# Kernel optimization log

Measured on AMD Instinct MI355X. Metric: run time of the kernel, lower is better.

## Reference

```python
import jax, jax.numpy as jnp
import numpy as np

B, H, W, C = 32, 56, 56, 256
WS = 7            # window size (hard-coded 49=7*7 in original topk modules)
NH = 8            # num heads
HD = C // NH      # head dim = 32
KCH = HD // 2     # channel top-k = 16
KSPT = 28         # spatial top-k
N = WS * WS       # 49 tokens per window
SCALE = HD ** -0.5
MLP_H = 4 * C

def _rel_index(ws):
    coords = np.stack(np.meshgrid(np.arange(ws), np.arange(ws), indexing='ij')).reshape(2, -1)
    rc = (coords[:, :, None] - coords[:, None, :]).transpose(1, 2, 0).astype(np.int64)
    rc[:, :, 0] += ws - 1
    rc[:, :, 1] += ws - 1
    rc[:, :, 0] *= 2 * ws - 1
    return jnp.asarray(rc.sum(-1))  # (N, N)

REL_IDX = _rel_index(WS)

def setup_inputs():
    key = jax.random.key(0)
    ks = jax.random.split(key, 10)
    p = lambda k, shp: jax.random.normal(k, shp, jnp.float32) * 0.02
    return dict(
        x=jax.random.normal(ks[0], (B, H * W, C), jnp.float32),
        norm1_g=jnp.ones((C,), jnp.float32), norm1_b=jnp.zeros((C,), jnp.float32),
        wq=p(ks[1], (C, C)), bq=jnp.zeros((C,), jnp.float32),
        wk=p(ks[2], (C // 2, C // 2)), bk=jnp.zeros((C // 2,), jnp.float32),
        wv=p(ks[3], (C, C)), bv=jnp.zeros((C,), jnp.float32),
        wproj=p(ks[4], (C, C)), bproj=jnp.zeros((C,), jnp.float32),
        wch=p(ks[5], (2 * HD, HD)), bch=jnp.zeros((HD,), jnp.float32),
        rpb_table=p(ks[6], ((2 * WS - 1) ** 2, NH)),
        norm2_g=jnp.ones((C,), jnp.float32), norm2_b=jnp.zeros((C,), jnp.float32),
        w1=p(ks[7], (C, MLP_H)), b1=jnp.zeros((MLP_H,), jnp.float32),
        w2=p(ks[8], (MLP_H, C)), b2=jnp.zeros((C,), jnp.float32),
    )

def _ln(x, g, b):
    mu = x.mean(-1, keepdims=True)
    var = x.var(-1, keepdims=True)
    return (x - mu) / jnp.sqrt(var + 1e-5) * g + b

def reference(x, norm1_g, norm1_b, wq, bq, wk, bk, wv, bv, wproj, bproj,
              wch, bch, rpb_table, norm2_g, norm2_b, w1, b1, w2, b2):
    shortcut = x
    xn = _ln(x, norm1_g, norm1_b).reshape(B, H, W, C)
    # window partition -> (Bw, N, C)
    xw = xn.reshape(B, H // WS, WS, W // WS, WS, C).transpose(0, 1, 3, 2, 4, 5).reshape(-1, N, C)
    Bw = xw.shape[0]
    q = xw @ wq + bq                                                    # (Bw, N, C)
    qh = q.reshape(Bw, N, NH, HD).transpose(0, 2, 1, 3).reshape(Bw * NH, N, HD)
    # ---- channel top-k (ChannelTopk) ----
    feat = jnp.concatenate([qh.mean(1), qh.max(1)], axis=-1)            # (Bn, 2*HD)
    score = jax.nn.softmax(jax.nn.gelu(feat @ wch + bch, approximate=False), axis=1)
    _, cidx = jax.lax.top_k(score, KCH)
    cidx = jnp.sort(cidx, axis=-1)                                      # sorted channel indices
    qcha = jnp.take_along_axis(qh, cidx[:, None, :], axis=2)            # (Bn, N, KCH)
    qcha1 = qcha.reshape(Bw, NH, N, KCH).transpose(0, 2, 1, 3).reshape(Bw, N, C // 2)
    k = qcha1 @ wk + bk                                                 # (Bw, N, C/2)
    # ---- relative position bias ----
    rpb = rpb_table[REL_IDX.reshape(-1)].reshape(N, N, NH).transpose(2, 0, 1)  # (NH, N, N)
    # ---- spatial top-k (SptialTopk) ----
    _, sidx = jax.lax.top_k(qh.mean(-1), KSPT)
    sidx = jnp.sort(sidx, axis=-1)                                      # (Bn, KSPT)
    qal = jnp.take_along_axis(qcha, sidx[:, :, None], axis=1)           # (Bn, KSPT, KCH)
    vsel = jnp.take_along_axis(qh, sidx[:, :, None], axis=1)            # (Bn, KSPT, HD)
    sidx_h = sidx.reshape(Bw, NH, KSPT)
    yal = jnp.take_along_axis(
        jnp.broadcast_to(rpb[None], (Bw, NH, N, N)),
        jnp.broadcast_to(sidx_h[:, :, None, :], (Bw, NH, N, KSPT)), axis=-1)  # (Bw, NH, N, KSPT)
    # ---- attention ----
    v = vsel.reshape(Bw, NH, KSPT, HD).transpose(0, 2, 1, 3).reshape(Bw, KSPT, C)
    v = (v @ wv + bv).reshape(Bw, KSPT, NH, HD).transpose(0, 2, 1, 3)   # (Bw, NH, KSPT, HD)
    qspt = (qal * SCALE).reshape(Bw, NH, KSPT, KCH)
    kh = k.reshape(Bw, N, NH, KCH).transpose(0, 2, 1, 3)                # (Bw, NH, N, KCH)
    attn = jnp.einsum('bnqc,bnkc->bnqk', kh, qspt) + yal                # (Bw, NH, N, KSPT)
    gate = jax.nn.sigmoid(attn.mean(-1))                                # (Bw, NH, N)
    attn = jax.nn.softmax(attn, axis=-1)
    o = jnp.einsum('bnqk,bnkd->bnqd', attn, v) * gate[..., None]        # (Bw, NH, N, HD)
    o = o.transpose(0, 2, 1, 3).reshape(Bw, N, C)
    o = o @ wproj + bproj
    # window reverse -> (B, L, C)
    xr = o.reshape(B, H // WS, W // WS, WS, WS, C).transpose(0, 1, 3, 2, 4, 5).reshape(B, H * W, C)
    x = shortcut + xr
    h = jax.nn.gelu(_ln(x, norm2_g, norm2_b) @ w1 + b1, approximate=False)
    return x + h @ w2 + b2
```

## Files before the change

### kernel.cpp

```cpp
#include <hip/hip_runtime.h>
#include <hip/hip_bf16.h>
#include <cmath>

#define CC 256
#define WSZ 7
#define WWD_ 56
#define NHD 8
#define HDIM 32
#define KCHN 16
#define KSP 28
#define NTOK 49
#define NWIN 2048
#define NBH 16384
#define LL 3136
#define MTOK 100352
#define MLPH 1024
#define SCALE_Q 0.17677669529663689f

typedef float floatx4 __attribute__((ext_vector_type(4)));
typedef __bf16 bf16x8_t __attribute__((ext_vector_type(8)));

__device__ __forceinline__ float gelu_f(float x) {
    return 0.5f * x * (1.0f + erff(x * 0.7071067811865475f));
}

__device__ __forceinline__ void lds_dma16(const void* g, void* l) {
    __builtin_amdgcn_global_load_lds((__attribute__((address_space(1))) void*)(void*)g,
                                     (__attribute__((address_space(3))) void*)l, 16, 0, 0);
}

__global__ __launch_bounds__(64) void ln_stats_k(const float* __restrict__ x,
                                                 float* __restrict__ mu,
                                                 float* __restrict__ rs) {
    int row = blockIdx.x;
    int lane = threadIdx.x;
    float4 v = reinterpret_cast<const float4*>(x + (size_t)row * CC)[lane];
    float s = v.x + v.y + v.z + v.w;
    float s2 = v.x * v.x + v.y * v.y + v.z * v.z + v.w * v.w;
#pragma unroll
    for (int off = 32; off > 0; off >>= 1) {
        s += __shfl_down(s, off);
        s2 += __shfl_down(s2, off);
    }
    if (lane == 0) {
        float m = s * (1.0f / CC);
        float var = s2 * (1.0f / CC) - m * m;
        mu[row] = m;
        rs[row] = rsqrtf(var + 1e-5f);
    }
}

struct GP {
    const float* W;
    const float* bias;
    float* C;
    int N, K;
    const float* x;
    const float* mu;
    const float* rs;
    const float* g;
    const float* be;
};

__global__ __launch_bounds__(256, 6) void gemm_q_k(GP p) {
    __shared__ __align__(16) float As[16][68];
    __shared__ __align__(16) float Bs[16][128];
    const int bm = blockIdx.x * 64;
    const int bn = blockIdx.y * 128;
    const int t = threadIdx.x;
    const int tx = t & 31;
    const int ty = t >> 5;
    const int w = t >> 6;

    const int ar = t >> 2;
    const int ak = (t & 3) * 4;

    const int r = bm + ar;
    int bwi = r / NTOK, n = r - bwi * NTOK;
    int b = bwi >> 6, rem = bwi & 63;
    int hw = rem >> 3, ww = rem & 7;
    int i0 = n / WSZ, j0 = n - i0 * WSZ;
    size_t grow = (size_t)b * LL + (size_t)(hw * WSZ + i0) * WWD_ + (ww * WSZ + j0);
    const float m = p.mu[grow], rsg = p.rs[grow];
    const float* xrow = p.x + grow * CC + ak;
    const float* gl = p.g + ak;
    const float* bl = p.be + ak;

    float acc[8][4] = {};

    for (int k0 = 0; k0 < CC; k0 += 16) {
        {
            float4 xv = *reinterpret_cast<const float4*>(xrow + k0);
            float4 gv = *reinterpret_cast<const float4*>(gl + k0);
            float4 bv = *reinterpret_cast<const float4*>(bl + k0);
            As[ak + 0][ar] = (xv.x - m) * rsg * gv.x + bv.x;
            As[ak + 1][ar] = (xv.y - m) * rsg * gv.y + bv.y;
            As[ak + 2][ar] = (xv.z - m) * rsg * gv.z + bv.z;
            As[ak + 3][ar] = (xv.w - m) * rsg * gv.w + bv.w;
        }
#pragma unroll
        for (int j = 0; j < 2; ++j) {
            const int c = j * 256 + t;
            const float* gp = p.W + (size_t)(k0 + (c >> 5)) * CC + bn + (c & 31) * 4;
            lds_dma16(gp, (char*)&Bs[0][0] + j * 4096 + w * 1024);
        }
        __syncthreads();
#pragma unroll
        for (int kk = 0; kk < 16; ++kk) {
            float a[8], bb[4];
            *(float4*)&a[0] = *(const float4*)&As[kk][ty * 8];
            *(float4*)&a[4] = *(const float4*)&As[kk][ty * 8 + 4];
            *(float4*)&bb[0] = *(const float4*)&Bs[kk][tx * 4];
#pragma unroll
            for (int i = 0; i < 8; ++i)
#pragma unroll
                for (int j = 0; j < 4; ++j) acc[i][j] = fmaf(a[i], bb[j], acc[i][j]);
        }
        __syncthreads();
    }

    float bj[4];
#pragma unroll
    for (int j = 0; j < 4; ++j) bj[j] = p.bias[bn + tx * 4 + j];
#pragma unroll
    for (int i = 0; i < 8; ++i) {
        const int row = bm + ty * 8 + i;
        float4 o = {acc[i][0] + bj[0], acc[i][1] + bj[1], acc[i][2] + bj[2], acc[i][3] + bj[3]};
        *reinterpret_cast<float4*>(p.C + (size_t)row * CC + bn + tx * 4) = o;
    }
}

struct MG {
    const __hip_bfloat16* A;
    const __hip_bfloat16* B;
    const float* bias;
    int N, K;
    float* Cf;
    __hip_bfloat16* Cb;
    const float* resid;
    int row0;
};

template <int EPI>
__global__ __launch_bounds__(256) void mgemm_k(MG p) {
    __shared__ __align__(16) __hip_bfloat16 As[2][128 * 32];
    __shared__ __align__(16) __hip_bfloat16 Bs[2][128 * 32];
    const int bm = blockIdx.x * 128;
    const int bn = blockIdx.y * 128;
    const int t = threadIdx.x;
    const int lane = t & 63;
    const int w = t >> 6;
    const int wm = (w & 1) * 64;
    const int wn = (w >> 1) * 64;
    const int fr = lane & 15;
    const int fk = (lane >> 4) * 8;

    const int m0 = t >> 2, m1 = (t + 256) >> 2;
    const int kc = (t & 3) * 8;
    const __hip_bfloat16* a0 = p.A + (size_t)(bm + m0) * p.K + kc;
    const __hip_bfloat16* a1 = p.A + (size_t)(bm + m1) * p.K + kc;
    const __hip_bfloat16* b0 = p.B + (size_t)(bn + m0) * p.K + kc;
    const __hip_bfloat16* b1 = p.B + (size_t)(bn + m1) * p.K + kc;

    auto stage = [&](int buf, int k0) {
        lds_dma16(a0 + k0, &As[buf][w * 512]);
        lds_dma16(a1 + k0, &As[buf][2048 + w * 512]);
        lds_dma16(b0 + k0, &Bs[buf][w * 512]);
        lds_dma16(b1 + k0, &Bs[buf][2048 + w * 512]);
    };

    floatx4 acc[4][4] = {};

    stage(0, 0);
    __syncthreads();
    int cur = 0;
    for (int k0 = 0; k0 < p.K; k0 += 32) {
        if (k0 + 32 < p.K) stage(cur ^ 1, k0 + 32);
        bf16x8_t af[4], bf[4];
#pragma unroll
        for (int i = 0; i < 4; ++i)
            af[i] = *(const bf16x8_t*)&As[cur][(wm + i * 16 + fr) * 32 + fk];
#pragma unroll
        for (int j = 0; j < 4; ++j)
            bf[j] = *(const bf16x8_t*)&Bs[cur][(wn + j * 16 + fr) * 32 + fk];
#pragma unroll
        for (int i = 0; i < 4; ++i)
#pragma unroll
            for (int j = 0; j < 4; ++j)
                acc[i][j] = __builtin_amdgcn_mfma_f32_16x16x32_bf16(af[i], bf[j], acc[i][j], 0, 0, 0);
        __syncthreads();
        cur ^= 1;
    }

    float bj[4];
#pragma unroll
    for (int j = 0; j < 4; ++j) bj[j] = p.bias[bn + wn + j * 16 + fr];
#pragma unroll
    for (int i = 0; i < 4; ++i) {
#pragma unroll
        for (int r = 0; r < 4; ++r) {
            const int m = bm + wm + i * 16 + (lane >> 4) * 4 + r;
#pragma unroll
            for (int j = 0; j < 4; ++j) {
                const int n = bn + wn + j * 16 + fr;
                float v = acc[i][j][r] + bj[j];
                if constexpr (EPI == 0) {
                    p.Cb[(size_t)m * p.N + n] = __float2bfloat16(v);
                } else if constexpr (EPI == 1) {
                    int bwi = m / NTOK, nn = m - bwi * NTOK;
                    int b = bwi >> 6, rem = bwi & 63;
                    int hw = rem >> 3, wwp = rem & 7;
                    int ii = nn / WSZ, jj = nn - ii * WSZ;
                    size_t oidx = ((size_t)b * LL + (size_t)(hw * WSZ + ii) * WWD_ + (wwp * WSZ + jj)) * CC + n;
                    p.Cf[oidx] = v + p.resid[oidx];
                } else if constexpr (EPI == 2) {
                    p.Cb[(size_t)m * p.N + n] = __float2bfloat16(gelu_f(v));
                } else {
                    size_t gr = (size_t)(m + p.row0);
                    p.Cf[gr * p.N + n] = v + p.resid[gr * p.N + n];
                }
            }
        }
    }
}

__global__ __launch_bounds__(256) void wt_k(const float* __restrict__ W,
                                            __hip_bfloat16* __restrict__ Wt, int K, int N) {
    int g = blockIdx.x * 256 + threadIdx.x;
    if (g >= K * N) return;
    int n = g / K, kk = g - n * K;
    Wt[g] = __float2bfloat16(W[(size_t)kk * N + n]);
}

__global__ __launch_bounds__(64) void topk_k(const float* __restrict__ q,
                                             const float* __restrict__ wch,
                                             const float* __restrict__ bch,
                                             short* __restrict__ cidx,
                                             short* __restrict__ sidx) {
    int bnh = blockIdx.x;
    int bwi = bnh >> 3, h = bnh & 7;
    int lane = threadIdx.x;
    __shared__ float tile[NTOK][HDIM + 1];
    __shared__ float feat[2 * HDIM];
    __shared__ float score[HDIM];
    __shared__ float rowm[NTOK];
    const float* qbase = q + ((size_t)bwi * NTOK) * CC + h * HDIM;
    for (int idx = lane; idx < NTOK * HDIM; idx += 64) {
        int n = idx >> 5, d = idx & 31;
        tile[n][d] = qbase[(size_t)n * CC + d];
    }
    __syncthreads();
    if (lane < HDIM) {
        float s = 0.f, mx = -INFINITY;
        for (int n = 0; n < NTOK; ++n) {
            float v = tile[n][lane];
            s += v;
            mx = fmaxf(mx, v);
        }
        feat[lane] = s * (1.0f / NTOK);
        feat[HDIM + lane] = mx;
    }
    if (lane < NTOK) {
        float s = 0.f;
        for (int d = 0; d < HDIM; ++d) s += tile[lane][d];
        rowm[lane] = s;
    }
    __syncthreads();
    if (lane < HDIM) {
        float s = bch[lane];
        for (int j = 0; j < 2 * HDIM; ++j) s += feat[j] * wch[j * HDIM + lane];
        score[lane] = gelu_f(s);
    }
    __syncthreads();
    {
        bool sel = false;
        if (lane < HDIM) {
            float sv = score[lane];
            int rank = 0;
            for (int j = 0; j < HDIM; ++j) {
                float oj = score[j];
                rank += (oj > sv) || (oj == sv && j < lane);
            }
            sel = rank < KCHN;
        }
        unsigned long long m = __ballot(sel);
        if (sel) {
            int pos = __popcll(m & ((1ull << lane) - 1ull));
            cidx[(size_t)bnh * KCHN + pos] = (short)lane;
        }
    }
    {
        bool sel = false;
        if (lane < NTOK) {
            float sv = rowm[lane];
            int rank = 0;
            for (int j = 0; j < NTOK; ++j) {
                float oj = rowm[j];
                rank += (oj > sv) || (oj == sv && j < lane);
            }
            sel = rank < KSP;
        }
        unsigned long long m = __ballot(sel);
        if (sel) {
            int pos = __popcll(m & ((1ull << lane) - 1ull));
            sidx[(size_t)bnh * KSP + pos] = (short)lane;
        }
    }
}

__global__ __launch_bounds__(256) void gather_ch_k(const float* __restrict__ q,
                                                   const short* __restrict__ cidx,
                                                   __hip_bfloat16* __restrict__ ak) {
    int g = blockIdx.x * 256 + threadIdx.x;
    int r = g >> 7, kk = g & 127;
    int bwi = r / NTOK;
    int hp = kk >> 4, c = kk & 15;
    int ci = cidx[((size_t)(bwi * NHD + hp)) * KCHN + c];
    ak[g] = __float2bfloat16(q[(size_t)r * CC + hp * HDIM + ci]);
}

__global__ __launch_bounds__(256) void gather_sp_k(const float* __restrict__ q,
                                                   const short* __restrict__ sidx,
                                                   __hip_bfloat16* __restrict__ av) {
    int g = blockIdx.x * 256 + threadIdx.x;
    int rr = g >> 8, c = g & 255;
    int bwi = rr / KSP, s = rr - bwi * KSP;
    int tok = sidx[((size_t)(bwi * NHD + (c >> 5))) * KSP + s];
    av[g] = __float2bfloat16(q[((size_t)(bwi * NTOK + tok)) * CC + c]);
}

__global__ __launch_bounds__(64) void attn_k(const float* __restrict__ q,
                                             const __hip_bfloat16* __restrict__ kb,
                                             const __hip_bfloat16* __restrict__ vb,
                                             const short* __restrict__ cidx,
                                             const short* __restrict__ sidx,
                                             const float* __restrict__ rpb,
                                             __hip_bfloat16* __restrict__ ob) {
    int bnh = blockIdx.x;
    int bwi = bnh >> 3, h = bnh & 7;
    int lane = threadIdx.x;
    __shared__ float kh_s[NTOK][KCHN + 1];
    __shared__ float qs_s[KSP][KCHN];
    __shared__ float v_s[KSP][HDIM];
    __shared__ int sidx_s[KSP];
    __shared__ int cidx_s[KCHN];
    if (lane < KSP) sidx_s[lane] = sidx[(size_t)bnh * KSP + lane];
    if (lane < KCHN) cidx_s[lane] = cidx[(size_t)bnh * KCHN + lane];
    for (int idx = lane; idx < NTOK * KCHN; idx += 64) {
        int n = idx >> 4, c = idx & 15;
        kh_s[n][c] = __bfloat162float(kb[((size_t)bwi * NTOK + n) * (NHD * KCHN) + h * KCHN + c]);
    }
    for (int idx = lane; idx < KSP * HDIM; idx += 64) {
        int s = idx >> 5, d = idx & 31;
        v_s[s][d] = __bfloat162float(vb[((size_t)bwi * KSP + s) * CC + h * HDIM + d]);
    }
    __syncthreads();
    for (int idx = lane; idx < KSP * KCHN; idx += 64) {
        int s = idx >> 4, c = idx & 15;
        qs_s[s][c] = q[((size_t)bwi * NTOK + sidx_s[s]) * CC + h * HDIM + cidx_s[c]] * SCALE_Q;
    }
    __syncthreads();
    if (lane < NTOK) {
        int i1 = lane / WSZ, j1 = lane - i1 * WSZ;
        float a[KSP];
        float msum = 0.f;
#pragma unroll
        for (int s = 0; s < KSP; ++s) {
            float dot = 0.f;
#pragma unroll
            for (int c = 0; c < KCHN; ++c) dot += kh_s[lane][c] * qs_s[s][c];
            int m = sidx_s[s];
            int i2 = m / WSZ, j2 = m - i2 * WSZ;
            float bias = rpb[(size_t)((i1 - i2 + 6) * 13 + (j1 - j2 + 6)) * NHD + h];
            a[s] = dot + bias;
            msum += a[s];
        }
        float gate = 1.0f / (1.0f + expf(-msum * (1.0f / KSP)));
        float mx = -INFINITY;
#pragma unroll
        for (int s = 0; s < KSP; ++s) mx = fmaxf(mx, a[s]);
        float sum = 0.f;
#pragma unroll
        for (int s = 0; s < KSP; ++s) {
            a[s] = expf(a[s] - mx);
            sum += a[s];
        }
        float inv = gate / sum;
        __hip_bfloat16* orow = ob + ((size_t)bwi * NTOK + lane) * CC + h * HDIM;
#pragma unroll
        for (int d = 0; d < HDIM; ++d) {
            float od = 0.f;
#pragma unroll
            for (int s = 0; s < KSP; ++s) od += a[s] * v_s[s][d];
            orow[d] = __float2bfloat16(od * inv);
        }
    }
}

__global__ __launch_bounds__(64) void ln2_k(const float* __restrict__ x2,
                                            const float* __restrict__ g,
                                            const float* __restrict__ b,
                                            __hip_bfloat16* __restrict__ a2) {
    int row = blockIdx.x;
    int lane = threadIdx.x;
    float4 v = reinterpret_cast<const float4*>(x2 + (size_t)row * CC)[lane];
    float s = v.x + v.y + v.z + v.w;
    float s2 = v.x * v.x + v.y * v.y + v.z * v.z + v.w * v.w;
#pragma unroll
    for (int off = 1; off < 64; off <<= 1) {
        s += __shfl_xor(s, off);
        s2 += __shfl_xor(s2, off);
    }
    float m = s * (1.0f / CC);
    float rsg = rsqrtf(s2 * (1.0f / CC) - m * m + 1e-5f);
    float4 gv = reinterpret_cast<const float4*>(g)[lane];
    float4 bv = reinterpret_cast<const float4*>(b)[lane];
    __hip_bfloat16* orow = a2 + (size_t)row * CC + lane * 4;
    orow[0] = __float2bfloat16((v.x - m) * rsg * gv.x + bv.x);
    orow[1] = __float2bfloat16((v.y - m) * rsg * gv.y + bv.y);
    orow[2] = __float2bfloat16((v.z - m) * rsg * gv.z + bv.z);
    orow[3] = __float2bfloat16((v.w - m) * rsg * gv.w + bv.w);
}

extern "C" void kernel_launch(void* const* d_in, const int* in_sizes, int n_in,
                              void* d_out, int out_size, void* d_ws, size_t ws_size,
                              hipStream_t stream) {
    const float* x   = (const float*)d_in[0];
    const float* n1g = (const float*)d_in[1];
    const float* n1b = (const float*)d_in[2];
    const float* wq  = (const float*)d_in[3];
    const float* bq  = (const float*)d_in[4];
    const float* wk  = (const float*)d_in[5];
    const float* bk  = (const float*)d_in[6];
    const float* wv  = (const float*)d_in[7];
    const float* bv  = (const float*)d_in[8];
    const float* wpj = (const float*)d_in[9];
    const float* bpj = (const float*)d_in[10];
    const float* wch = (const float*)d_in[11];
    const float* bch = (const float*)d_in[12];
    const float* rpb = (const float*)d_in[13];
    const float* n2g = (const float*)d_in[14];
    const float* n2b = (const float*)d_in[15];
    const float* w1  = (const float*)d_in[16];
    const float* b1  = (const float*)d_in[17];
    const float* w2  = (const float*)d_in[18];
    const float* b2  = (const float*)d_in[19];
    float* out = (float*)d_out;

    char* wsb = (char*)d_ws;
    float* qb            = (float*)wsb;
    __hip_bfloat16* g1   = (__hip_bfloat16*)(wsb + 102760448);
    __hip_bfloat16* g2   = (__hip_bfloat16*)(wsb + 128450560);
    __hip_bfloat16* ob   = g1;
    __hip_bfloat16* kb   = (__hip_bfloat16*)(wsb + 157810688);
    __hip_bfloat16* vb   = (__hip_bfloat16*)(wsb + 183500800);
    float* mu1           = (float*)(wsb + 212860928);
    float* rs1           = mu1 + MTOK;
    short* cidx          = (short*)(wsb + 213663744);
    short* sidx          = (short*)(wsb + 214188032);
    __hip_bfloat16* wkt  = (__hip_bfloat16*)(wsb + 215105536);
    __hip_bfloat16* wvt  = (__hip_bfloat16*)(wsb + 215138304);
    __hip_bfloat16* wpt  = (__hip_bfloat16*)(wsb + 215269376);
    __hip_bfloat16* w1t  = (__hip_bfloat16*)(wsb + 215400448);
    __hip_bfloat16* w2t  = (__hip_bfloat16*)(wsb + 215924736);
    __hip_bfloat16* a2   = (__hip_bfloat16*)qb;
    __hip_bfloat16* hb   = (__hip_bfloat16*)(wsb + 102760448);
    if (ws_size < 216449024ULL) return;

    wt_k<<<(128 * 128 + 255) / 256, 256, 0, stream>>>(wk, wkt, 128, 128);
    wt_k<<<(256 * 256 + 255) / 256, 256, 0, stream>>>(wv, wvt, 256, 256);
    wt_k<<<(256 * 256 + 255) / 256, 256, 0, stream>>>(wpj, wpt, 256, 256);
    wt_k<<<(256 * 1024 + 255) / 256, 256, 0, stream>>>(w1, w1t, 256, 1024);
    wt_k<<<(1024 * 256 + 255) / 256, 256, 0, stream>>>(w2, w2t, 1024, 256);

    ln_stats_k<<<MTOK, 64, 0, stream>>>(x, mu1, rs1);

    GP p{};
    p.W = wq; p.bias = bq; p.C = qb; p.N = CC; p.K = CC;
    p.x = x; p.mu = mu1; p.rs = rs1; p.g = n1g; p.be = n1b;
    gemm_q_k<<<dim3(MTOK / 64, 2), 256, 0, stream>>>(p);

    topk_k<<<NBH, 64, 0, stream>>>(qb, wch, bch, cidx, sidx);

    gather_ch_k<<<MTOK * 128 / 256, 256, 0, stream>>>(qb, cidx, g1);
    MG m{};
    m.A = g1; m.B = wkt; m.bias = bk; m.N = 128; m.K = 128; m.Cb = kb;
    mgemm_k<0><<<dim3(MTOK / 128, 1), 256, 0, stream>>>(m);

    gather_sp_k<<<NWIN * KSP * 256 / 256, 256, 0, stream>>>(qb, sidx, g2);
    m = MG{};
    m.A = g2; m.B = wvt; m.bias = bv; m.N = CC; m.K = CC; m.Cb = vb;
    mgemm_k<0><<<dim3(NWIN * KSP / 128, 2), 256, 0, stream>>>(m);

    attn_k<<<NBH, 64, 0, stream>>>(qb, kb, vb, cidx, sidx, rpb, ob);

    m = MG{};
    m.A = ob; m.B = wpt; m.bias = bpj; m.N = CC; m.K = CC; m.Cf = out; m.resid = x;
    mgemm_k<1><<<dim3(MTOK / 128, 2), 256, 0, stream>>>(m);

    ln2_k<<<MTOK, 64, 0, stream>>>(out, n2g, n2b, a2);

    const int CHUNK = MTOK / 2;
    for (int c = 0; c < 2; ++c) {
        int start = c * CHUNK;
        m = MG{};
        m.A = a2 + (size_t)start * CC; m.B = w1t; m.bias = b1;
        m.N = MLPH; m.K = CC; m.Cb = hb;
        mgemm_k<2><<<dim3(CHUNK / 128, MLPH / 128), 256, 0, stream>>>(m);

        m = MG{};
        m.A = hb; m.B = w2t; m.bias = b2; m.N = CC; m.K = MLPH;
        m.Cf = out; m.resid = out; m.row0 = start;
        mgemm_k<3><<<dim3(CHUNK / 128, CC / 128), 256, 0, stream>>>(m);
    }
}
```

Before: 1.189 ms.

## Process all heads of a window per block in attention kernel with vectorized loads

The attention kernel now runs one 512-thread block per window, with one wavefront per head, in place of one 64-thread block per (window, head). K and V tiles for the whole window are loaded with 16-byte vector loads into shared memory, K is kept in registers, and the PV product and the bf16 output stores are vectorized four values at a time. The aim is fewer tiny blocks, coalesced global loads and fewer scalar LDS/global accesses. The cost is larger shared memory per block and more registers, which may lower occupancy.

```diff
diff --git a/kernel.cpp b/kernel.cpp
--- a/kernel.cpp
+++ b/kernel.cpp
@@ -329,47 +329,83 @@
     av[g] = __float2bfloat16(q[((size_t)(bwi * NTOK + tok)) * CC + c]);
 }
 
-__global__ __launch_bounds__(64) void attn_k(const float* __restrict__ q,
-                                             const __hip_bfloat16* __restrict__ kb,
-                                             const __hip_bfloat16* __restrict__ vb,
-                                             const short* __restrict__ cidx,
-                                             const short* __restrict__ sidx,
-                                             const float* __restrict__ rpb,
-                                             __hip_bfloat16* __restrict__ ob) {
-    int bnh = blockIdx.x;
-    int bwi = bnh >> 3, h = bnh & 7;
-    int lane = threadIdx.x;
-    __shared__ float kh_s[NTOK][KCHN + 1];
-    __shared__ float qs_s[KSP][KCHN];
-    __shared__ float v_s[KSP][HDIM];
-    __shared__ int sidx_s[KSP];
-    __shared__ int cidx_s[KCHN];
-    if (lane < KSP) sidx_s[lane] = sidx[(size_t)bnh * KSP + lane];
-    if (lane < KCHN) cidx_s[lane] = cidx[(size_t)bnh * KCHN + lane];
-    for (int idx = lane; idx < NTOK * KCHN; idx += 64) {
-        int n = idx >> 4, c = idx & 15;
-        kh_s[n][c] = __bfloat162float(kb[((size_t)bwi * NTOK + n) * (NHD * KCHN) + h * KCHN + c]);
-    }
-    for (int idx = lane; idx < KSP * HDIM; idx += 64) {
-        int s = idx >> 5, d = idx & 31;
-        v_s[s][d] = __bfloat162float(vb[((size_t)bwi * KSP + s) * CC + h * HDIM + d]);
+__global__ __launch_bounds__(512) void attn_k(const float* __restrict__ q,
+                                              const __hip_bfloat16* __restrict__ kb,
+                                              const __hip_bfloat16* __restrict__ vb,
+                                              const short* __restrict__ cidx,
+                                              const short* __restrict__ sidx,
+                                              const float* __restrict__ rpb,
+                                              __hip_bfloat16* __restrict__ ob) {
+    const int bwi = blockIdx.x;
+    const int tid = threadIdx.x;
+    const int h = tid >> 6;
+    const int lane = tid & 63;
+    __shared__ __hip_bfloat16 kh_s[NTOK][132];
+    __shared__ float v_s[KSP][256];
+    __shared__ float qs_s[NHD][KSP][KCHN];
+    __shared__ int sidx_s[NHD][KSP];
+    __shared__ int cidx_s[NHD][KCHN];
+
+    if (tid < NHD * KSP) {
+        sidx_s[tid / KSP][tid % KSP] = sidx[(size_t)bwi * NHD * KSP + tid];
+    } else if (tid < NHD * KSP + NHD * KCHN) {
+        int u = tid - NHD * KSP;
+        cidx_s[u / KCHN][u % KCHN] = cidx[(size_t)bwi * NHD * KCHN + u];
+    }
+    {
+        const __hip_bfloat16* kbase = kb + (size_t)bwi * NTOK * (NHD * KCHN);
+        for (int ch = tid; ch < NTOK * 16; ch += 512) {
+            int n = ch >> 4, c8 = (ch & 15) * 8;
+            uint4 u = *(const uint4*)(kbase + n * 128 + c8);
+            uint2* dst = (uint2*)&kh_s[n][c8];
+            dst[0] = make_uint2(u.x, u.y);
+            dst[1] = make_uint2(u.z, u.w);
+        }
+    }
+    {
+        const __hip_bfloat16* vbase = vb + (size_t)bwi * KSP * CC;
+        for (int ch = tid; ch < KSP * 32; ch += 512) {
+            int n = ch >> 5, c8 = (ch & 31) * 8;
+            union { uint4 u; __hip_bfloat16 b[8]; } tt;
+            tt.u = *(const uint4*)(vbase + n * CC + c8);
+#pragma unroll
+            for (int j = 0; j < 8; ++j) v_s[n][c8 + j] = __bfloat162float(tt.b[j]);
+        }
     }
     __syncthreads();
-    for (int idx = lane; idx < KSP * KCHN; idx += 64) {
-        int s = idx >> 4, c = idx & 15;
-        qs_s[s][c] = q[((size_t)bwi * NTOK + sidx_s[s]) * CC + h * HDIM + cidx_s[c]] * SCALE_Q;
+#pragma unroll
+    for (int k = 0; k < 7; ++k) {
+        int idx = tid + k * 512;
+        int hh = idx / (KSP * KCHN), r = idx - hh * (KSP * KCHN);
+        int s = r >> 4, c = r & 15;
+        qs_s[hh][s][c] =
+            q[((size_t)bwi * NTOK + sidx_s[hh][s]) * CC + hh * HDIM + cidx_s[hh][c]] * SCALE_Q;
     }
     __syncthreads();
+
     if (lane < NTOK) {
+        float khr[16];
+        {
+            const uint* kp = (const uint*)&kh_s[lane][h * KCHN];
+#pragma unroll
+            for (int j = 0; j < 8; ++j) {
+                uint u = kp[j];
+                __hip_bfloat162 b2 = *(__hip_bfloat162*)&u;
+                float2 f = __bfloat1622float2(b2);
+                khr[2 * j] = f.x;
+                khr[2 * j + 1] = f.y;
+            }
+        }
         int i1 = lane / WSZ, j1 = lane - i1 * WSZ;
         float a[KSP];
         float msum = 0.f;
 #pragma unroll
         for (int s = 0; s < KSP; ++s) {
+            const float* qrow = &qs_s[h][s][0];
             float dot = 0.f;
 #pragma unroll
-            for (int c = 0; c < KCHN; ++c) dot += kh_s[lane][c] * qs_s[s][c];
-            int m = sidx_s[s];
+            for (int c = 0; c < KCHN; ++c) dot += khr[c] * qrow[c];
+            int m = sidx_s[h][s];
             int i2 = m / WSZ, j2 = m - i2 * WSZ;
             float bias = rpb[(size_t)((i1 - i2 + 6) * 13 + (j1 - j2 + 6)) * NHD + h];
             a[s] = dot + bias;
@@ -386,13 +422,31 @@
             sum += a[s];
         }
         float inv = gate / sum;
+        float4 ov[8];
+#pragma unroll
+        for (int d4 = 0; d4 < 8; ++d4) ov[d4] = float4{0.f, 0.f, 0.f, 0.f};
+#pragma unroll
+        for (int s = 0; s < KSP; ++s) {
+            const float4* vrow = (const float4*)&v_s[s][h * HDIM];
+            float as = a[s];
+#pragma unroll
+            for (int d4 = 0; d4 < 8; ++d4) {
+                float4 vv = vrow[d4];
+                ov[d4].x += as * vv.x;
+                ov[d4].y += as * vv.y;
+                ov[d4].z += as * vv.z;
+                ov[d4].w += as * vv.w;
+            }
+        }
         __hip_bfloat16* orow = ob + ((size_t)bwi * NTOK + lane) * CC + h * HDIM;
 #pragma unroll
-        for (int d = 0; d < HDIM; ++d) {
-            float od = 0.f;
-#pragma unroll
-            for (int s = 0; s < KSP; ++s) od += a[s] * v_s[s][d];
-            orow[d] = __float2bfloat16(od * inv);
+        for (int d4 = 0; d4 < 8; ++d4) {
+            union { __hip_bfloat16 b[4]; uint2 u; } pk;
+            pk.b[0] = __float2bfloat16(ov[d4].x * inv);
+            pk.b[1] = __float2bfloat16(ov[d4].y * inv);
+            pk.b[2] = __float2bfloat16(ov[d4].z * inv);
+            pk.b[3] = __float2bfloat16(ov[d4].w * inv);
+            *(uint2*)(orow + d4 * 4) = pk.u;
         }
     }
 }
@@ -492,7 +546,7 @@
     m.A = g2; m.B = wvt; m.bias = bv; m.N = CC; m.K = CC; m.Cb = vb;
     mgemm_k<0><<<dim3(NWIN * KSP / 128, 2), 256, 0, stream>>>(m);
 
-    attn_k<<<NBH, 64, 0, stream>>>(qb, kb, vb, cidx, sidx, rpb, ob);
+    attn_k<<<NWIN, 512, 0, stream>>>(qb, kb, vb, cidx, sidx, rpb, ob);
 
     m = MG{};
     m.A = ob; m.B = wpt; m.bias = bpj; m.N = CC; m.K = CC; m.Cf = out; m.resid = x;
```

Result: faster. 1.051 ms (-11.7%).
